# Optimization experiments

Hardware: AMD Instinct MI355X
Metric: run time of the kernel (lower is better)

The kernel has to match this reference:

```python
import jax, jax.numpy as jnp
import numpy as np

B, L, D, C, DEPTH = 2, 1024, 256, 16, 4
N = L // C  # chunks per sequence
EPS = 1.1920929e-07  # torch RMSNorm default eps = finfo(fp32).eps


def rmsnorm(x, w):
    return x * jax.lax.rsqrt(jnp.mean(x * x, axis=-1, keepdims=True) + EPS) * w


def mlp_apply(ws, x):
    # titans MLP: x @ W0, then silu -> @ W1, ... (works for batched [*,d,d] weights too)
    for i, w in enumerate(ws):
        if i:
            x = jax.nn.silu(x)
        x = x @ w
    return x


def setup_inputs() -> dict:
    key = jax.random.key(0)
    ks = jax.random.split(key, 10)
    s = np.float32(1.0 / np.sqrt(D))
    return {
        "seq": jax.random.normal(ks[0], (B, L, D), jnp.float32),
        "w_store_norm": jnp.ones((D,), jnp.float32),
        "w_retrieve_norm": jnp.ones((D,), jnp.float32),
        "w_post_norm": jnp.ones((D,), jnp.float32),
        "Wq": jax.random.normal(ks[1], (D, D), jnp.float32) * s,
        "Wkv": jax.random.normal(ks[2], (D, 2 * D), jnp.float32) * s,
        "w_adapt": jax.random.normal(ks[3], (D,), jnp.float32) * s,
        "w_mom": jax.random.normal(ks[4], (D,), jnp.float32) * s,
        "w_decay": jax.random.normal(ks[5], (D,), jnp.float32) * s,
        "W0": jax.random.normal(ks[6], (D, D), jnp.float32) * s,
        "W1": jax.random.normal(ks[7], (D, D), jnp.float32) * s,
        "W2": jax.random.normal(ks[8], (D, D), jnp.float32) * s,
        "W3": jax.random.normal(ks[9], (D, D), jnp.float32) * s,
    }


def _forward(seq, w_store_norm, w_retrieve_norm, w_post_norm, Wq, Wkv,
             w_adapt, w_mom, w_decay, W0, W1, W2, W3):
    ws = (W0, W1, W2, W3)

    # ---------------- store_memories ----------------
    sn = rmsnorm(seq, w_store_norm)                      # [B,L,D]; L already multiple of C
    cm = sn.reshape(B, N, C, D).mean(axis=2)             # per-chunk mean [B,N,D]
    adaptive_lr = jax.nn.sigmoid(cm @ w_adapt)           # [B,N]
    adaptive_mom = jax.nn.sigmoid(cm @ w_mom)[..., None]   # [B,N,1]
    decay = jax.nn.sigmoid(cm @ w_decay)[..., None]        # [B,N,1]

    kv = sn @ Wkv                                        # [B,L,2D]
    keys = kv[..., :D].reshape(B * N, C, D)
    vals = kv[..., D:].reshape(B * N, C, D)

    def chunk_loss(params, k, v):
        pred = mlp_apply(params, k)                      # [C,D]
        return jnp.sum(jnp.mean((pred - v) ** 2, axis=-1))

    # per-chunk grads wrt the 4 MLP weights (past weights are zero at init)
    grads = jax.vmap(jax.grad(chunk_loss), in_axes=(None, 0, 0))(ws, keys, vals)
    g = jnp.stack(grads, axis=1).reshape(B, N, DEPTH * D * D)  # packed 'b n *'
    surprise = -adaptive_lr[..., None] * g               # [B,N,P]

    def op(l, r):
        al, xl = l
        ar, xr = r
        return (al * ar, xl * ar + xr)                   # x_t = a_t*x_{t-1} + b_t

    _, momentum = jax.lax.associative_scan(op, (adaptive_mom, surprise), axis=1)
    _, updates = jax.lax.associative_scan(op, (1.0 - decay, momentum), axis=1)
    upd = updates.reshape(B, N, DEPTH, D, D)

    # per-chunk fast weights: base params + cumulative update
    fast_ws = tuple((w + upd[:, :, i]).reshape(B * N, D, D) for i, w in enumerate(ws))

    # ---------------- retrieve_memories ----------------
    rn = rmsnorm(seq, w_retrieve_norm)[:, C - 1:]        # [B, L-C+1, D]
    rn = jnp.pad(rn, ((0, 0), (0, C - 1), (0, 0)))       # pad back up to [B,L,D]
    q = (rn @ Wq).reshape(B * N, C, D)
    out = mlp_apply(fast_ws, q).reshape(B, L, D)         # batched fast-weight MLP
    out = rmsnorm(out, w_post_norm)
    out = jnp.pad(out, ((0, 0), (C - 1, 0), (0, 0)))[:, :-(C - 1)]  # shift by C-1
    return out


def reference(seq, w_store_norm, w_retrieve_norm, w_post_norm, Wq, Wkv,
              w_adapt, w_mom, w_decay, W0, W1, W2, W3):
    return _forward(seq, w_store_norm, w_retrieve_norm, w_post_norm, Wq, Wkv,
                    w_adapt, w_mom, w_decay, W0, W1, W2, W3)
```

## Files before the change

### kernel.cpp

```cpp
#include <hip/hip_runtime.h>
#include <hip/hip_bf16.h>

typedef __attribute__((ext_vector_type(8)))  short s8v;
typedef __attribute__((ext_vector_type(4)))  float f4v;
typedef _Float16 h4 __attribute__((ext_vector_type(4)));
typedef __attribute__((ext_vector_type(4))) unsigned short u4v;

constexpr int NCn  = 128;
constexpr int DDn  = 65536;
constexpr int XP   = 264;
constexpr float EPSf = 1.1920929e-07f;

__device__ __forceinline__ float sigm(float x){ return 1.0f/(1.0f + expf(-x)); }
__device__ __forceinline__ float silu_(float x){ return x * sigm(x); }
__device__ __forceinline__ float dsilu_(float x){ float s = sigm(x); return s*(1.0f + x*(1.0f - s)); }

__device__ __forceinline__ unsigned short f2b(float x){
    __hip_bfloat16 b = __float2bfloat16(x);
    unsigned short u; __builtin_memcpy(&u, &b, 2); return u;
}
__device__ __forceinline__ float b2f(unsigned short u){
    __hip_bfloat16 b; __builtin_memcpy(&b, &u, 2); return __bfloat162float(b);
}
__device__ __forceinline__ h4 ldh4(const unsigned short* p){
    h4 r; __builtin_memcpy(&r, p, 8); return r;
}

__device__ __forceinline__ int fidx(int row, int col){
    return (((row >> 4)*8 + (col >> 5))*4 + ((col >> 3) & 3))*128 + (row & 15)*8 + (col & 7);
}

__device__ __forceinline__ float block_sum(float v, float* red){
    #pragma unroll
    for (int off = 32; off; off >>= 1) v += __shfl_down(v, off, 64);
    if ((threadIdx.x & 63) == 0) red[threadIdx.x >> 6] = v;
    __syncthreads();
    float r = red[0] + red[1] + red[2] + red[3];
    __syncthreads();
    return r;
}

__global__ __launch_bounds__(256) void ktw(const float* __restrict__ Wq,
        const float* __restrict__ Wkv, const float* __restrict__ W0,
        const float* __restrict__ W1, const float* __restrict__ W2,
        const float* __restrict__ W3, unsigned short* __restrict__ WTb,
        unsigned short* __restrict__ WqTb, unsigned short* __restrict__ WkvTb,
        unsigned short* __restrict__ Wb){
    int z = blockIdx.z;
    if (z >= 6){
        const float* S = (z==6)?W1:(z==7)?W2:W3;
        size_t idx = (((size_t)blockIdx.y*8 + blockIdx.x)*256 + threadIdx.x)*2;
        float2 v = *(const float2*)(S + idx);
        ushort2 u; u.x = f2b(v.x); u.y = f2b(v.y);
        int row = (int)(idx >> 8), col = (int)(idx & 255);
        *(ushort2*)(Wb + (size_t)(z-6)*DDn + fidx(row, col)) = u;
        return;
    }
    __shared__ float tl[32][33];
    if (z != 5 && blockIdx.y >= 8) return;
    const float* S; unsigned short* T; int C;
    if (z < 4){ S = (z==0)?W0:(z==1)?W1:(z==2)?W2:W3; T = WTb + (size_t)z*DDn; C = 256; }
    else if (z == 4){ S = Wq; T = WqTb; C = 256; }
    else { S = Wkv; T = WkvTb; C = 512; }
    int k0 = blockIdx.x*32, j0 = blockIdx.y*32;
    int tx = threadIdx.x & 31, ty = threadIdx.x >> 5;
    #pragma unroll
    for (int p = 0; p < 4; ++p)
        tl[ty + 8*p][tx] = S[(size_t)(k0 + ty + 8*p)*C + j0 + tx];
    __syncthreads();
    #pragma unroll
    for (int p = 0; p < 4; ++p){
        int r = j0 + ty + 8*p, k = k0 + tx;
        T[fidx(r, k)] = f2b(tl[tx][ty + 8*p]);
    }
}

__global__ __launch_bounds__(256) void knorm(const float* __restrict__ seq,
        const float* __restrict__ wsn, const float* __restrict__ wrn,
        unsigned short* __restrict__ snb, unsigned short* __restrict__ snF,
        unsigned short* __restrict__ rnF){
    __shared__ float red[4];
    int t = blockIdx.x, d = threadIdx.x;
    int b = t >> 10, tl = t & 1023, g = t >> 4, c = tl & 15;
    float x = seq[(size_t)t*256 + d];
    float ss = block_sum(x*x, red);
    float xr = x * rsqrtf(ss*(1.f/256.f) + EPSf);
    unsigned short sv = f2b(xr*wsn[d]);
    snb[(size_t)g*4096 + c*256 + d] = sv;
    snF[(size_t)g*4096 + fidx(c, d)] = sv;
    if (tl >= 15){
        int tl2 = tl - 15, g2 = b*64 + (tl2 >> 4), c2 = tl2 & 15;
        rnF[(size_t)g2*4096 + fidx(c2, d)] = f2b(xr*wrn[d]);
    }
    if (tl >= 1009)
        rnF[(size_t)g*4096 + fidx(c, d)] = 0;
}

__global__ __launch_bounds__(1024, 1) void kfb(const unsigned short* __restrict__ snb,
        const unsigned short* __restrict__ snF,
        const unsigned short* __restrict__ WkvTb, const unsigned short* __restrict__ WTb,
        const unsigned short* __restrict__ Wb,
        const float* __restrict__ wa, const float* __restrict__ wm,
        const float* __restrict__ wdk,
        float* __restrict__ momg, float* __restrict__ decg,
        unsigned short* __restrict__ XT, unsigned short* __restrict__ GT){
    __shared__ unsigned short xl[4][16][XP];
    __shared__ unsigned short Gs[16][XP];
    __shared__ float red3[16][4];
    int tid = threadIdx.x, w = tid >> 6, lane = tid & 63;
    int m16 = lane & 15, q16 = lane >> 4;
    int g = blockIdx.x;
    int n0 = w*16;
    size_t fb = (size_t)w*4096 + q16*128 + m16*8;

    s8v af[8];
    const unsigned short* arow = snF + (size_t)g*4096 + q16*128 + m16*8;
    #pragma unroll
    for (int i = 0; i < 8; ++i) af[i] = *(const s8v*)(arow + i*512);

    float sc;
    {
        int d2 = tid & 255, qt = tid >> 8;
        float a = 0.f;
        #pragma unroll
        for (int c = 0; c < 4; ++c)
            a += b2f(snb[(size_t)g*4096 + (qt*4 + c)*256 + d2]);
        float cm = a * (1.f/16.f);
        float s0 = cm*wa[d2], s1 = cm*wm[d2], s2 = cm*wdk[d2];
        #pragma unroll
        for (int off = 32; off; off >>= 1){
            s0 += __shfl_down(s0, off, 64);
            s1 += __shfl_down(s1, off, 64);
            s2 += __shfl_down(s2, off, 64);
        }
        if (lane == 0){ red3[w][0] = s0; red3[w][1] = s1; red3[w][2] = s2; }
        __syncthreads();
        float da = 0.f, dm = 0.f, dc = 0.f;
        #pragma unroll
        for (int i = 0; i < 16; ++i){
            da += red3[i][0]; dm += red3[i][1]; dc += red3[i][2];
        }
        sc = -2.f * sigm(da) * (1.f/256.f);
        if (tid == 0){ momg[g] = sigm(dm); decg[g] = sigm(dc); }
    }

    s8v bpre[8];
    #pragma unroll
    for (int i = 0; i < 8; ++i) bpre[i] = *(const s8v*)(WTb + fb + i*512);

    f4v vacc;
    {
        f4v ka = {0.f,0.f,0.f,0.f}, va = {0.f,0.f,0.f,0.f};
        const unsigned short* brK = WkvTb + fb;
        const unsigned short* brV = WkvTb + (size_t)DDn + fb;
        #pragma unroll
        for (int i = 0; i < 8; ++i){
            s8v bK = *(const s8v*)(brK + i*512);
            s8v bV = *(const s8v*)(brV + i*512);
            ka = __builtin_amdgcn_mfma_f32_16x16x32_bf16(af[i], bK, ka, 0, 0, 0);
            va = __builtin_amdgcn_mfma_f32_16x16x32_bf16(af[i], bV, va, 0, 0, 0);
        }
        vacc = va;
        #pragma unroll
        for (int r = 0; r < 4; ++r) xl[0][4*q16 + r][n0 + m16] = f2b(ka[r]);
    }

    f4v hreg[3];
    #pragma unroll
    for (int l = 0; l < 3; ++l){
        __syncthreads();
        s8v xa[8];
        #pragma unroll
        for (int i = 0; i < 8; ++i)
            xa[i] = *(const s8v*)(&xl[l][m16][q16*8 + i*32]);
        s8v bcur[8];
        #pragma unroll
        for (int i = 0; i < 8; ++i) bcur[i] = bpre[i];
        const unsigned short* nxt = WTb + (size_t)(l+1)*DDn + fb;
        #pragma unroll
        for (int i = 0; i < 8; ++i) bpre[i] = *(const s8v*)(nxt + i*512);
        f4v acc = {0.f,0.f,0.f,0.f};
        #pragma unroll
        for (int i = 0; i < 8; ++i)
            acc = __builtin_amdgcn_mfma_f32_16x16x32_bf16(xa[i], bcur[i], acc, 0, 0, 0);
        hreg[l] = acc;
        #pragma unroll
        for (int r = 0; r < 4; ++r)
            xl[l+1][4*q16 + r][n0 + m16] = f2b(silu_(acc[r]));
    }
    __syncthreads();

    {
        int d = tid & 255, qt = tid >> 8;
        #pragma unroll
        for (int l = 0; l < 4; ++l){
            h4 v;
            #pragma unroll
            for (int j = 0; j < 4; ++j)
                v[j] = (_Float16)b2f(xl[l][qt*4 + j][d]);
            *(h4*)(XT + (((size_t)l*128 + g)*256 + d)*16 + qt*4) = v;
        }
    }

    {
        s8v xa[8];
        #pragma unroll
        for (int i = 0; i < 8; ++i)
            xa[i] = *(const s8v*)(&xl[3][m16][q16*8 + i*32]);
        s8v bcur[8];
        #pragma unroll
        for (int i = 0; i < 8; ++i) bcur[i] = bpre[i];
        const unsigned short* nxt = Wb + (size_t)2*DDn + fb;
        #pragma unroll
        for (int i = 0; i < 8; ++i) bpre[i] = *(const s8v*)(nxt + i*512);
        f4v acc = {0.f,0.f,0.f,0.f};
        #pragma unroll
        for (int i = 0; i < 8; ++i)
            acc = __builtin_amdgcn_mfma_f32_16x16x32_bf16(xa[i], bcur[i], acc, 0, 0, 0);
        #pragma unroll
        for (int r = 0; r < 4; ++r)
            Gs[4*q16 + r][n0 + m16] = f2b(sc * (acc[r] - vacc[r]));
    }
    __syncthreads();
    {
        int d = tid & 255, qt = tid >> 8;
        h4 v;
        #pragma unroll
        for (int j = 0; j < 4; ++j)
            v[j] = (_Float16)b2f(Gs[qt*4 + j][d]);
        *(h4*)(GT + (((size_t)3*128 + g)*256 + d)*16 + qt*4) = v;
    }

    #pragma unroll
    for (int l = 3; l >= 1; --l){
        s8v gfa[8];
        #pragma unroll
        for (int i = 0; i < 8; ++i)
            gfa[i] = *(const s8v*)(&Gs[m16][q16*8 + i*32]);
        s8v bcur[8];
        #pragma unroll
        for (int i = 0; i < 8; ++i) bcur[i] = bpre[i];
        if (l > 1){
            const unsigned short* nxt = Wb + (size_t)(l-2)*DDn + fb;
            #pragma unroll
            for (int i = 0; i < 8; ++i) bpre[i] = *(const s8v*)(nxt + i*512);
        }
        f4v acc = {0.f,0.f,0.f,0.f};
        #pragma unroll
        for (int i = 0; i < 8; ++i)
            acc = __builtin_amdgcn_mfma_f32_16x16x32_bf16(gfa[i], bcur[i], acc, 0, 0, 0);
        f4v gn;
        #pragma unroll
        for (int r = 0; r < 4; ++r)
            gn[r] = acc[r] * dsilu_(hreg[l-1][r]);
        __syncthreads();
        #pragma unroll
        for (int r = 0; r < 4; ++r)
            Gs[4*q16 + r][n0 + m16] = f2b(gn[r]);
        __syncthreads();
        {
            int d = tid & 255, qt = tid >> 8;
            h4 v;
            #pragma unroll
            for (int j = 0; j < 4; ++j)
                v[j] = (_Float16)b2f(Gs[qt*4 + j][d]);
            *(h4*)(GT + (((size_t)(l-1)*128 + g)*256 + d)*16 + qt*4) = v;
        }
    }
}

__global__ __launch_bounds__(64, 1) void kck(const unsigned short* __restrict__ XT,
        const unsigned short* __restrict__ GT, const float* __restrict__ momg,
        const float* __restrict__ decg, unsigned short* __restrict__ ucpb){
    int lane = threadIdx.x;
    int m16 = lane & 15, q16 = lane >> 4;
    int rt = blockIdx.x, ct = blockIdx.y, bl = blockIdx.z;
    int b = bl >> 2, l = bl & 3;
    int dr = rt*16 + m16;
    int dc = ct*16 + m16;
    const unsigned short* Gb  = GT + ((size_t)l*128 + b*64)*4096 + (size_t)dr*16 + q16*4;
    const unsigned short* Xb2 = XT + ((size_t)l*128 + b*64)*4096 + (size_t)dc*16 + q16*4;
    int col = ct*16 + m16;
    int fo0 = ((rt*8 + (col >> 5))*4 + ((col >> 3) & 3))*128 + (4*q16)*8 + (col & 7);
    f4v us = {0.f,0.f,0.f,0.f}, ms = {0.f,0.f,0.f,0.f};
    #pragma unroll 4
    for (int n = 0; n < 64; ++n){
        float mo = momg[b*64 + n], de = 1.f - decg[b*64 + n];
        h4 a  = ldh4(Gb  + (size_t)n*4096);
        h4 xb = ldh4(Xb2 + (size_t)n*4096);
        f4v z = {0.f,0.f,0.f,0.f};
        f4v s = __builtin_amdgcn_mfma_f32_16x16x16f16(a, xb, z, 0, 0, 0);
        size_t cb = ((size_t)bl*64 + n)*65536;
        #pragma unroll
        for (int r = 0; r < 4; ++r){
            float mn = mo*ms[r] + s[r];
            float un = de*us[r] + mn;
            ms[r] = mn; us[r] = un;
            ucpb[cb + fo0 + r*8] = f2b(un);
        }
    }
}

__global__ __launch_bounds__(1024, 1) void kretr(const unsigned short* __restrict__ rnF,
        const unsigned short* __restrict__ WqTb, const unsigned short* __restrict__ WTb,
        const unsigned short* __restrict__ ucpb, const float* __restrict__ wpost,
        float* __restrict__ out){
    __shared__ unsigned short xc[2][16][XP];
    __shared__ float red[16][16];
    __shared__ float rs[16];
    int tid = threadIdx.x, w = tid >> 6, lane = tid & 63;
    int m16 = lane & 15, q16 = lane >> 4;
    int g = blockIdx.x;
    int b = g >> 6, nl = g & 63;
    int n0 = w*16;
    size_t fb = (size_t)w*4096 + q16*128 + m16*8;
    size_t afb = (size_t)q16*128 + m16*8;

    {
        s8v a[8];
        const unsigned short* ar = rnF + (size_t)g*4096 + afb;
        #pragma unroll
        for (int i = 0; i < 8; ++i) a[i] = *(const s8v*)(ar + i*512);
        f4v acc = {0.f,0.f,0.f,0.f};
        const unsigned short* br = WqTb + fb;
        #pragma unroll
        for (int i = 0; i < 8; ++i){
            s8v bb = *(const s8v*)(br + i*512);
            acc = __builtin_amdgcn_mfma_f32_16x16x32_bf16(a[i], bb, acc, 0, 0, 0);
        }
        #pragma unroll
        for (int r = 0; r < 4; ++r) xc[0][4*q16 + r][n0 + m16] = f2b(acc[r]);
    }
    __syncthreads();

    f4v hacc;
    for (int l = 0; l < 4; ++l){
        s8v xa[8];
        #pragma unroll
        for (int i = 0; i < 8; ++i)
            xa[i] = *(const s8v*)(&xc[l & 1][m16][q16*8 + i*32]);
        const unsigned short* br = WTb + (size_t)l*DDn + fb;
        const unsigned short* bu = ucpb + ((size_t)(b*4 + l)*64 + nl)*65536 + fb;
        f4v acc = {0.f,0.f,0.f,0.f};
        #pragma unroll
        for (int i = 0; i < 8; ++i){
            s8v w0 = *(const s8v*)(br + i*512);
            s8v u0 = *(const s8v*)(bu + i*512);
            acc = __builtin_amdgcn_mfma_f32_16x16x32_bf16(xa[i], w0, acc, 0, 0, 0);
            acc = __builtin_amdgcn_mfma_f32_16x16x32_bf16(xa[i], u0, acc, 0, 0, 0);
        }
        hacc = acc;
        if (l < 3){
            #pragma unroll
            for (int r = 0; r < 4; ++r)
                xc[(l + 1) & 1][4*q16 + r][n0 + m16] = f2b(silu_(hacc[r]));
            __syncthreads();
        }
    }

    float part[4];
    #pragma unroll
    for (int r = 0; r < 4; ++r) part[r] = hacc[r]*hacc[r];
    #pragma unroll
    for (int off = 1; off < 16; off <<= 1)
        #pragma unroll
        for (int r = 0; r < 4; ++r) part[r] += __shfl_xor(part[r], off, 64);
    if (m16 == 0)
        #pragma unroll
        for (int r = 0; r < 4; ++r) red[w][4*q16 + r] = part[r];
    __syncthreads();
    if (tid < 16){
        float s = 0.f;
        #pragma unroll
        for (int i = 0; i < 16; ++i) s += red[i][tid];
        rs[tid] = rsqrtf(s*(1.f/256.f) + EPSf);
    }
    __syncthreads();
    {
        int d = n0 + m16;
        float wp = wpost[d];
        #pragma unroll
        for (int r = 0; r < 4; ++r){
            int c = 4*q16 + r;
            int tp = nl*16 + c + 15;
            if (tp < 1024)
                out[((size_t)b*1024 + tp)*256 + d] = hacc[r]*rs[c]*wp;
        }
    }
    if (nl == 0){
        for (int idx = tid; idx < 15*256; idx += 1024)
            out[(size_t)b*262144 + idx] = 0.f;
    }
}

extern "C" void kernel_launch(void* const* d_in, const int* in_sizes, int n_in,
                              void* d_out, int out_size, void* d_ws, size_t ws_size,
                              hipStream_t stream) {
    const float* seq     = (const float*)d_in[0];
    const float* w_store = (const float*)d_in[1];
    const float* w_retr  = (const float*)d_in[2];
    const float* w_post  = (const float*)d_in[3];
    const float* Wq      = (const float*)d_in[4];
    const float* Wkv     = (const float*)d_in[5];
    const float* w_adapt = (const float*)d_in[6];
    const float* w_mom   = (const float*)d_in[7];
    const float* w_decay = (const float*)d_in[8];
    const float* W0      = (const float*)d_in[9];
    const float* W1      = (const float*)d_in[10];
    const float* W2      = (const float*)d_in[11];
    const float* W3      = (const float*)d_in[12];

    float* momg  = (float*)d_ws;
    float* decg  = momg + NCn;
    unsigned short* snb   = (unsigned short*)(decg + NCn + 32);
    unsigned short* snF   = snb   + (size_t)NCn*4096;
    unsigned short* rnF   = snF   + (size_t)NCn*4096;
    unsigned short* WTb   = rnF   + (size_t)NCn*4096;
    unsigned short* Wb    = WTb   + 4*(size_t)DDn;
    unsigned short* WqTb  = Wb    + 3*(size_t)DDn;
    unsigned short* WkvTb = WqTb  + (size_t)DDn;
    unsigned short* XT    = WkvTb + 2*(size_t)DDn;
    unsigned short* GT    = XT    + (size_t)4*NCn*4096;
    unsigned short* ucpb  = GT    + (size_t)4*NCn*4096;

    ktw   <<<dim3(8, 16, 9),  256,  0, stream>>>(Wq, Wkv, W0, W1, W2, W3,
                                                 WTb, WqTb, WkvTb, Wb);
    knorm <<<dim3(2048),      256,  0, stream>>>(seq, w_store, w_retr, snb, snF, rnF);
    kfb   <<<dim3(NCn),       1024, 0, stream>>>(snb, snF, WkvTb, WTb, Wb,
                                                 w_adapt, w_mom, w_decay,
                                                 momg, decg, XT, GT);
    kck   <<<dim3(16, 16, 8), 64,   0, stream>>>(XT, GT, momg, decg, ucpb);
    kretr <<<dim3(NCn),       1024, 0, stream>>>(rnF, WqTb, WTb, ucpb,
                                                 w_post, (float*)d_out);
}
```

Before: 147.2 us.

## Fuse RMSNorm into store and retrieve kernels, drop separate norm pass

Removes the standalone knorm kernel and computes the store RMSNorm inside kfb and the retrieve RMSNorm (with its C-1 shift and zero padding) inside kretr. Each wave normalizes one token row into shared memory, and the MFMA A fragments are then read from LDS instead of from precomputed global bf16 buffers. This saves a kernel launch and a global round trip of the normalized activations, at the cost of an extra barrier and LDS space. It also splits the fast-weight accumulator into separate base and update accumulators, which breaks the serial MFMA dependency chain.

```diff
diff --git a/kernel.cpp b/kernel.cpp
--- a/kernel.cpp
+++ b/kernel.cpp
@@ -28,16 +28,6 @@
 
 __device__ __forceinline__ int fidx(int row, int col){
     return (((row >> 4)*8 + (col >> 5))*4 + ((col >> 3) & 3))*128 + (row & 15)*8 + (col & 7);
-}
-
-__device__ __forceinline__ float block_sum(float v, float* red){
-    #pragma unroll
-    for (int off = 32; off; off >>= 1) v += __shfl_down(v, off, 64);
-    if ((threadIdx.x & 63) == 0) red[threadIdx.x >> 6] = v;
-    __syncthreads();
-    float r = red[0] + red[1] + red[2] + red[3];
-    __syncthreads();
-    return r;
 }
 
 __global__ __launch_bounds__(256) void ktw(const float* __restrict__ Wq,
@@ -75,35 +65,15 @@
     }
 }
 
-__global__ __launch_bounds__(256) void knorm(const float* __restrict__ seq,
-        const float* __restrict__ wsn, const float* __restrict__ wrn,
-        unsigned short* __restrict__ snb, unsigned short* __restrict__ snF,
-        unsigned short* __restrict__ rnF){
-    __shared__ float red[4];
-    int t = blockIdx.x, d = threadIdx.x;
-    int b = t >> 10, tl = t & 1023, g = t >> 4, c = tl & 15;
-    float x = seq[(size_t)t*256 + d];
-    float ss = block_sum(x*x, red);
-    float xr = x * rsqrtf(ss*(1.f/256.f) + EPSf);
-    unsigned short sv = f2b(xr*wsn[d]);
-    snb[(size_t)g*4096 + c*256 + d] = sv;
-    snF[(size_t)g*4096 + fidx(c, d)] = sv;
-    if (tl >= 15){
-        int tl2 = tl - 15, g2 = b*64 + (tl2 >> 4), c2 = tl2 & 15;
-        rnF[(size_t)g2*4096 + fidx(c2, d)] = f2b(xr*wrn[d]);
-    }
-    if (tl >= 1009)
-        rnF[(size_t)g*4096 + fidx(c, d)] = 0;
-}
-
-__global__ __launch_bounds__(1024, 1) void kfb(const unsigned short* __restrict__ snb,
-        const unsigned short* __restrict__ snF,
+__global__ __launch_bounds__(1024, 1) void kfb(const float* __restrict__ seq,
+        const float* __restrict__ wsn,
         const unsigned short* __restrict__ WkvTb, const unsigned short* __restrict__ WTb,
         const unsigned short* __restrict__ Wb,
         const float* __restrict__ wa, const float* __restrict__ wm,
         const float* __restrict__ wdk,
         float* __restrict__ momg, float* __restrict__ decg,
         unsigned short* __restrict__ XT, unsigned short* __restrict__ GT){
+    __shared__ unsigned short xs[16][XP];
     __shared__ unsigned short xl[4][16][XP];
     __shared__ unsigned short Gs[16][XP];
     __shared__ float red3[16][4];
@@ -113,10 +83,19 @@
     int n0 = w*16;
     size_t fb = (size_t)w*4096 + q16*128 + m16*8;
 
-    s8v af[8];
-    const unsigned short* arow = snF + (size_t)g*4096 + q16*128 + m16*8;
-    #pragma unroll
-    for (int i = 0; i < 8; ++i) af[i] = *(const s8v*)(arow + i*512);
+    {
+        const float4 xv = *(const float4*)(seq + ((size_t)g*16 + w)*256 + lane*4);
+        const float4 wv = *(const float4*)(wsn + lane*4);
+        float ssq = xv.x*xv.x + xv.y*xv.y + xv.z*xv.z + xv.w*xv.w;
+        #pragma unroll
+        for (int off = 32; off; off >>= 1) ssq += __shfl_xor(ssq, off, 64);
+        float s2 = rsqrtf(ssq*(1.f/256.f) + EPSf);
+        u4v sv;
+        sv[0] = f2b(xv.x*s2*wv.x); sv[1] = f2b(xv.y*s2*wv.y);
+        sv[2] = f2b(xv.z*s2*wv.z); sv[3] = f2b(xv.w*s2*wv.w);
+        *(u4v*)(&xs[w][lane*4]) = sv;
+    }
+    __syncthreads();
 
     float sc;
     {
@@ -124,7 +103,7 @@
         float a = 0.f;
         #pragma unroll
         for (int c = 0; c < 4; ++c)
-            a += b2f(snb[(size_t)g*4096 + (qt*4 + c)*256 + d2]);
+            a += b2f(xs[qt*4 + c][d2]);
         float cm = a * (1.f/16.f);
         float s0 = cm*wa[d2], s1 = cm*wm[d2], s2 = cm*wdk[d2];
         #pragma unroll
@@ -143,6 +122,10 @@
         sc = -2.f * sigm(da) * (1.f/256.f);
         if (tid == 0){ momg[g] = sigm(dm); decg[g] = sigm(dc); }
     }
+
+    s8v af[8];
+    #pragma unroll
+    for (int i = 0; i < 8; ++i) af[i] = *(const s8v*)(&xs[m16][q16*8 + i*32]);
 
     s8v bpre[8];
     #pragma unroll
@@ -301,7 +284,8 @@
     }
 }
 
-__global__ __launch_bounds__(1024, 1) void kretr(const unsigned short* __restrict__ rnF,
+__global__ __launch_bounds__(1024, 1) void kretr(const float* __restrict__ seq,
+        const float* __restrict__ wrn,
         const unsigned short* __restrict__ WqTb, const unsigned short* __restrict__ WTb,
         const unsigned short* __restrict__ ucpb, const float* __restrict__ wpost,
         float* __restrict__ out){
@@ -314,13 +298,28 @@
     int b = g >> 6, nl = g & 63;
     int n0 = w*16;
     size_t fb = (size_t)w*4096 + q16*128 + m16*8;
-    size_t afb = (size_t)q16*128 + m16*8;
+
+    {
+        int p = nl*16 + w + 15;
+        u4v sv = {0,0,0,0};
+        if (p < 1024){
+            const float4 xv = *(const float4*)(seq + ((size_t)b*1024 + p)*256 + lane*4);
+            const float4 wv = *(const float4*)(wrn + lane*4);
+            float ssq = xv.x*xv.x + xv.y*xv.y + xv.z*xv.z + xv.w*xv.w;
+            #pragma unroll
+            for (int off = 32; off; off >>= 1) ssq += __shfl_xor(ssq, off, 64);
+            float s2 = rsqrtf(ssq*(1.f/256.f) + EPSf);
+            sv[0] = f2b(xv.x*s2*wv.x); sv[1] = f2b(xv.y*s2*wv.y);
+            sv[2] = f2b(xv.z*s2*wv.z); sv[3] = f2b(xv.w*s2*wv.w);
+        }
+        *(u4v*)(&xc[1][w][lane*4]) = sv;
+    }
+    __syncthreads();
 
     {
         s8v a[8];
-        const unsigned short* ar = rnF + (size_t)g*4096 + afb;
-        #pragma unroll
-        for (int i = 0; i < 8; ++i) a[i] = *(const s8v*)(ar + i*512);
+        #pragma unroll
+        for (int i = 0; i < 8; ++i) a[i] = *(const s8v*)(&xc[1][m16][q16*8 + i*32]);
         f4v acc = {0.f,0.f,0.f,0.f};
         const unsigned short* br = WqTb + fb;
         #pragma unroll
@@ -341,15 +340,16 @@
             xa[i] = *(const s8v*)(&xc[l & 1][m16][q16*8 + i*32]);
         const unsigned short* br = WTb + (size_t)l*DDn + fb;
         const unsigned short* bu = ucpb + ((size_t)(b*4 + l)*64 + nl)*65536 + fb;
-        f4v acc = {0.f,0.f,0.f,0.f};
+        f4v aW = {0.f,0.f,0.f,0.f}, aU = {0.f,0.f,0.f,0.f};
         #pragma unroll
         for (int i = 0; i < 8; ++i){
             s8v w0 = *(const s8v*)(br + i*512);
             s8v u0 = *(const s8v*)(bu + i*512);
-            acc = __builtin_amdgcn_mfma_f32_16x16x32_bf16(xa[i], w0, acc, 0, 0, 0);
-            acc = __builtin_amdgcn_mfma_f32_16x16x32_bf16(xa[i], u0, acc, 0, 0, 0);
-        }
-        hacc = acc;
+            aW = __builtin_amdgcn_mfma_f32_16x16x32_bf16(xa[i], w0, aW, 0, 0, 0);
+            aU = __builtin_amdgcn_mfma_f32_16x16x32_bf16(xa[i], u0, aU, 0, 0, 0);
+        }
+        #pragma unroll
+        for (int r = 0; r < 4; ++r) hacc[r] = aW[r] + aU[r];
         if (l < 3){
             #pragma unroll
             for (int r = 0; r < 4; ++r)
@@ -412,10 +412,7 @@
 
     float* momg  = (float*)d_ws;
     float* decg  = momg + NCn;
-    unsigned short* snb   = (unsigned short*)(decg + NCn + 32);
-    unsigned short* snF   = snb   + (size_t)NCn*4096;
-    unsigned short* rnF   = snF   + (size_t)NCn*4096;
-    unsigned short* WTb   = rnF   + (size_t)NCn*4096;
+    unsigned short* WTb   = (unsigned short*)(decg + NCn + 32);
     unsigned short* Wb    = WTb   + 4*(size_t)DDn;
     unsigned short* WqTb  = Wb    + 3*(size_t)DDn;
     unsigned short* WkvTb = WqTb  + (size_t)DDn;
@@ -425,11 +422,10 @@
 
     ktw   <<<dim3(8, 16, 9),  256,  0, stream>>>(Wq, Wkv, W0, W1, W2, W3,
                                                  WTb, WqTb, WkvTb, Wb);
-    knorm <<<dim3(2048),      256,  0, stream>>>(seq, w_store, w_retr, snb, snF, rnF);
-    kfb   <<<dim3(NCn),       1024, 0, stream>>>(snb, snF, WkvTb, WTb, Wb,
+    kfb   <<<dim3(NCn),       1024, 0, stream>>>(seq, w_store, WkvTb, WTb, Wb,
                                                  w_adapt, w_mom, w_decay,
                                                  momg, decg, XT, GT);
     kck   <<<dim3(16, 16, 8), 64,   0, stream>>>(XT, GT, momg, decg, ucpb);
-    kretr <<<dim3(NCn),       1024, 0, stream>>>(rnF, WqTb, WTb, ucpb,
+    kretr <<<dim3(NCn),       1024, 0, stream>>>(seq, w_retr, WqTb, WTb, ucpb,
                                                  w_post, (float*)d_out);
 }
```

After: 143.3 us. -2.6%, faster.
